# Kernel tuning notes

Measured on AMD Instinct MI355X. Metric: run time of the kernel, lower is better.

The kernel has to match this reference:

```python
import jax, jax.numpy as jnp
import numpy as np


def _pairwise_dist(x, y):
    # x: [B, N, D], y: [B, M, D] -> Euclidean distances [B, N, M]
    # numerical safety before sqrt.
    x2 = jnp.sum(x * x, axis=-1)            # [B, N]
    y2 = jnp.sum(y * y, axis=-1)            # [B, M]
    xy = jnp.einsum('bnd,bmd->bnm', x, y)   # [B, N, M]
    d2 = x2[:, :, None] + y2[:, None, :] - 2.0 * xy
    return jnp.sqrt(jnp.maximum(d2, 0.0))


def setup_inputs() -> dict:
    key = jax.random.key(0)
    k1, k2 = jax.random.split(key)
    B, N, M, D = 4, 8192, 8192, 3
    true_pos = jax.random.normal(k1, (B, N, D), dtype=jnp.float32)
    pred_pos = jax.random.normal(k2, (B, M, D), dtype=jnp.float32)
    return {"true_pos": true_pos, "pred_pos": pred_pos}


def reference(true_pos, pred_pos):
    dists = _pairwise_dist(true_pos.astype(jnp.float32),
                           pred_pos.astype(jnp.float32))  # [B, N, M]
    mins = jnp.min(dists, axis=2)        # [B, N] nearest pred for each true
    mins_seeds = jnp.min(dists, axis=1)  # [B, M] nearest true for each pred
    loss = jnp.mean(mins)
    loss_seeds = jnp.mean(mins_seeds)
    return (loss + loss_seeds, mins_seeds)
```

## Files before the change

### kernel.cpp

```cpp
#include <hip/hip_runtime.h>

typedef __attribute__((ext_vector_type(4)))  short bf16x4;
typedef __attribute__((ext_vector_type(16))) float f32x16;

#define TPB    256
#define NPTS   8192
#define NB     4
#define TOTPTS (NB * NPTS)
#define XWAVE  64
#define XBLK   (4 * XWAVE)
#define YTILE  1024
#define NTILES (YTILE / 32)
#define GXB    (NPTS / XBLK)
#define GYB    (NPTS / YTILE)
#define NSLICE (2 * NB)
#define WS2_FLOATS ((size_t)GYB * NSLICE * NPTS)
#define NPARTIAL ((2 * TOTPTS) / 64)


__device__ __forceinline__ short bfr(float f) {
    unsigned u = __float_as_uint(f);
    return (short)((u + 0x7FFFu + ((u >> 16) & 1u)) >> 16);
}
__device__ __forceinline__ float bf2f(short s) {
    return __uint_as_float(((unsigned)(unsigned short)s) << 16);
}

__global__ void __launch_bounds__(TPB, 1) nnmin_mfma(
        const float* __restrict__ T, const float* __restrict__ P,
        float* __restrict__ ws2)
{
    __shared__ bf16x4 sA[NTILES * 64];

    const int z   = blockIdx.z;
    const int dir = z >> 2;
    const int b   = z & 3;
    const float* Xb = (dir ? P : T) + (size_t)b * NPTS * 3;
    const float* Yb = (dir ? T : P) + (size_t)b * NPTS * 3;
    const int t     = threadIdx.x;
    const int l     = t & 63;
    const int w     = t >> 6;
    const int ybase = blockIdx.y * YTILE;
    const int xw    = blockIdx.x * XBLK + w * XWAVE;

    for (int p = t; p < YTILE; p += TPB) {
        const float* yp = Yb + (size_t)(ybase + p) * 3;
        float y0 = yp[0], y1 = yp[1], y2 = yp[2];
        short yh0 = bfr(y0); short yl0 = bfr(y0 - bf2f(yh0));
        short yh1 = bfr(y1); short yl1 = bfr(y1 - bf2f(yh1));
        short yh2 = bfr(y2); short yl2 = bfr(y2 - bf2f(yh2));
        float hy  = 0.5f * (y0 * y0 + y1 * y1 + y2 * y2);
        short hyh = bfr(hy); short hyl = bfr(hy - bf2f(hyh));
        int tile = p >> 5, m = p & 31;
        bf16x4 e0 = {yh0, yl0, yh1, yl1};
        bf16x4 e1 = {yh2, yl2, hyh, hyl};
        sA[tile * 64 + m]      = e0;
        sA[tile * 64 + 32 + m] = e1;
    }

    const int   kh  = l >> 5;
    const short ONE = 0x3F80;
    bf16x4 B[2];
#pragma unroll
    for (int f = 0; f < 2; ++f) {
        const float* xp = Xb + (size_t)(xw + f * 32 + (l & 31)) * 3;
        short h0 = bfr(-xp[0]);
        short h1 = bfr(-xp[1]);
        short h2 = bfr(-xp[2]);
        bf16x4 e;
        if (kh == 0) e = (bf16x4){h0, h0, h1, h1};
        else         e = (bf16x4){h2, h2, ONE, ONE};
        B[f] = e;
    }
    __syncthreads();

    f32x16 zero = {0.f};
    float rm[2][16];
#pragma unroll
    for (int f = 0; f < 2; ++f)
#pragma unroll
        for (int i = 0; i < 16; ++i) rm[f][i] = 3.0e38f;

#pragma unroll 2
    for (int tl = 0; tl < NTILES; tl += 2) {
        bf16x4 Aa = sA[(tl + 0) * 64 + l];
        bf16x4 Ab = sA[(tl + 1) * 64 + l];
#pragma unroll
        for (int f = 0; f < 2; ++f) {
            f32x16 da = __builtin_amdgcn_mfma_f32_32x32x8bf16_1k(Aa, B[f], zero, 0, 0, 0);
            f32x16 db = __builtin_amdgcn_mfma_f32_32x32x8bf16_1k(Ab, B[f], zero, 0, 0, 0);
#pragma unroll
            for (int i = 0; i < 16; ++i) {
                float ea = da[i], eb = db[i];
                asm("v_min3_f32 %0, %0, %1, %2"
                    : "+v"(rm[f][i]) : "v"(ea), "v"(eb));
            }
        }
    }

    float* o = ws2 + ((size_t)blockIdx.y * NSLICE + z) * NPTS;
#pragma unroll
    for (int f = 0; f < 2; ++f) {
        float v = rm[f][0];
#pragma unroll
        for (int i = 1; i < 16; ++i) v = fminf(v, rm[f][i]);
        v = fminf(v, __shfl_xor(v, 32, 64));
        if (l < 32) o[xw + f * 32 + l] = v;
    }
}

__global__ void __launch_bounds__(TPB) finalize_kernel(
        const float* __restrict__ ws2,
        const float* __restrict__ T, const float* __restrict__ P,
        float* __restrict__ out, float* __restrict__ partials)
{
    int i   = blockIdx.x * TPB + threadIdx.x;
    int dir = (i >= TOTPTS) ? 1 : 0;
    int idx = i - dir * TOTPTS;
    int b   = idx >> 13;
    int x   = idx & (NPTS - 1);

    const float* p0 = ws2 + (size_t)(dir * 4 + b) * NPTS + x;
    float m = 3.0e38f;
#pragma unroll
    for (int c = 0; c < GYB; ++c)
        m = fminf(m, p0[(size_t)c * NSLICE * NPTS]);

    const float* xp = (dir ? P : T) + ((size_t)b * NPTS + x) * 3;
    float a0 = bf2f(bfr(xp[0]));
    float a1 = bf2f(bfr(xp[1]));
    float a2 = bf2f(bfr(xp[2]));
    float hx = 0.5f * (a0 * a0 + a1 * a1 + a2 * a2);
    float d  = sqrtf(fmaxf(2.0f * (hx + m), 0.0f));
    if (dir) out[1 + idx] = d;

#pragma unroll
    for (int off = 32; off > 0; off >>= 1)
        d += __shfl_down(d, off, 64);
    if ((threadIdx.x & 63) == 0) partials[i >> 6] = d;
}

__global__ void scalar_kernel(const float* __restrict__ partials,
                              float* __restrict__ out) {
    int t = threadIdx.x;
    float s = 0.0f;
#pragma unroll
    for (int k = 0; k < NPARTIAL / 64; ++k)
        s += partials[t * (NPARTIAL / 64) + k];
#pragma unroll
    for (int off = 32; off > 0; off >>= 1)
        s += __shfl_down(s, off, 64);
    if (t == 0) out[0] = s * (1.0f / (float)TOTPTS);
}

extern "C" void kernel_launch(void* const* d_in, const int* in_sizes, int n_in,
                              void* d_out, int out_size, void* d_ws, size_t ws_size,
                              hipStream_t stream) {
    const float* truep = (const float*)d_in[0];
    const float* predp = (const float*)d_in[1];
    float* out = (float*)d_out;

    float* ws2      = (float*)d_ws;
    float* partials = ws2 + WS2_FLOATS;

    dim3 grid(GXB, GYB, 2 * NB);
    nnmin_mfma<<<grid, TPB, 0, stream>>>(truep, predp, ws2);

    finalize_kernel<<<(2 * TOTPTS) / TPB, TPB, 0, stream>>>(
        ws2, truep, predp, out, partials);
    scalar_kernel<<<1, 64, 0, stream>>>(partials, out);
}
```

Measured before the change: 81.04 us.

## Software-pipeline MFMA tiles against min3 tree reductions, collapse running minima

The inner loop is restructured so the MFMAs for the next tile are issued before the min reductions of the current tile's results, overlapping matrix-core latency with VALU work. Each MFMA output is reduced by a v_min3 tree into a single running minimum per fragment, replacing the 32 per-element accumulators and cutting register pressure. At the end the loop computes one extra wrapped tile, which is harmless because min is idempotent. The scalar reduction kernel also switches to a coalesced read pattern.

```diff
diff --git a/kernel.cpp b/kernel.cpp
--- a/kernel.cpp
+++ b/kernel.cpp
@@ -24,6 +24,21 @@
 }
 __device__ __forceinline__ float bf2f(short s) {
     return __uint_as_float(((unsigned)(unsigned short)s) << 16);
+}
+__device__ __forceinline__ float min3f(float a, float b, float c) {
+    float d;
+    asm("v_min3_f32 %0, %1, %2, %3" : "=v"(d) : "v"(a), "v"(b), "v"(c));
+    return d;
+}
+__device__ __forceinline__ void tree16(const f32x16& d, float& rm) {
+    float u0 = min3f(d[0],  d[1],  d[2]);
+    float u1 = min3f(d[3],  d[4],  d[5]);
+    float u2 = min3f(d[6],  d[7],  d[8]);
+    float u3 = min3f(d[9],  d[10], d[11]);
+    float u4 = min3f(d[12], d[13], d[14]);
+    float v0 = min3f(u0, u1, d[15]);
+    float v1 = min3f(u2, u3, u4);
+    asm("v_min3_f32 %0, %0, %1, %2" : "+v"(rm) : "v"(v0), "v"(v1));
 }
 
 __global__ void __launch_bounds__(TPB, 1) nnmin_mfma(
@@ -75,37 +90,36 @@
     __syncthreads();
 
     f32x16 zero = {0.f};
-    float rm[2][16];
-#pragma unroll
-    for (int f = 0; f < 2; ++f)
-#pragma unroll
-        for (int i = 0; i < 16; ++i) rm[f][i] = 3.0e38f;
+    float rm0 = 3.0e38f, rm1 = 3.0e38f;
 
-#pragma unroll 2
+    bf16x4 A0 = sA[l];
+    bf16x4 Ab = sA[64 + l];
+    f32x16 da = __builtin_amdgcn_mfma_f32_32x32x8bf16_1k(A0, B[0], zero, 0, 0, 0);
+    f32x16 db = __builtin_amdgcn_mfma_f32_32x32x8bf16_1k(A0, B[1], zero, 0, 0, 0);
+
+#pragma unroll 1
     for (int tl = 0; tl < NTILES; tl += 2) {
-        bf16x4 Aa = sA[(tl + 0) * 64 + l];
-        bf16x4 Ab = sA[(tl + 1) * 64 + l];
-#pragma unroll
-        for (int f = 0; f < 2; ++f) {
-            f32x16 da = __builtin_amdgcn_mfma_f32_32x32x8bf16_1k(Aa, B[f], zero, 0, 0, 0);
-            f32x16 db = __builtin_amdgcn_mfma_f32_32x32x8bf16_1k(Ab, B[f], zero, 0, 0, 0);
-#pragma unroll
-            for (int i = 0; i < 16; ++i) {
-                float ea = da[i], eb = db[i];
-                asm("v_min3_f32 %0, %0, %1, %2"
-                    : "+v"(rm[f][i]) : "v"(ea), "v"(eb));
-            }
-        }
+        bf16x4 An2 = sA[((tl + 2) & (NTILES - 1)) * 64 + l];
+        bf16x4 An3 = sA[((tl + 3) & (NTILES - 1)) * 64 + l];
+        f32x16 na = __builtin_amdgcn_mfma_f32_32x32x8bf16_1k(Ab, B[0], zero, 0, 0, 0);
+        f32x16 nb = __builtin_amdgcn_mfma_f32_32x32x8bf16_1k(Ab, B[1], zero, 0, 0, 0);
+        tree16(da, rm0);
+        tree16(db, rm1);
+        da = __builtin_amdgcn_mfma_f32_32x32x8bf16_1k(An2, B[0], zero, 0, 0, 0);
+        db = __builtin_amdgcn_mfma_f32_32x32x8bf16_1k(An2, B[1], zero, 0, 0, 0);
+        tree16(na, rm0);
+        tree16(nb, rm1);
+        Ab = An3;
     }
 
     float* o = ws2 + ((size_t)blockIdx.y * NSLICE + z) * NPTS;
-#pragma unroll
-    for (int f = 0; f < 2; ++f) {
-        float v = rm[f][0];
-#pragma unroll
-        for (int i = 1; i < 16; ++i) v = fminf(v, rm[f][i]);
-        v = fminf(v, __shfl_xor(v, 32, 64));
-        if (l < 32) o[xw + f * 32 + l] = v;
+    {
+        float v = fminf(rm0, __shfl_xor(rm0, 32, 64));
+        if (l < 32) o[xw + l] = v;
+    }
+    {
+        float v = fminf(rm1, __shfl_xor(rm1, 32, 64));
+        if (l < 32) o[xw + 32 + l] = v;
     }
 }
 
@@ -146,7 +160,7 @@
     float s = 0.0f;
 #pragma unroll
     for (int k = 0; k < NPARTIAL / 64; ++k)
-        s += partials[t * (NPARTIAL / 64) + k];
+        s += partials[t + 64 * k];
 #pragma unroll
     for (int off = 32; off > 0; off >>= 1)
         s += __shfl_down(s, off, 64);
```

Result: no change. 81.87 us (+1.0%).
